# Kernel tuning notes

Hardware: AMD Instinct MI355X
Metric: run time of the kernel (lower is better)

Reference implementation:

```python
import jax, jax.numpy as jnp
import numpy as np

LN_EPS = 1e-6  # flax.linen.LayerNorm default


def setup_inputs() -> dict:
    key = jax.random.key(0)
    ks = jax.random.split(key, 16)
    N_TOT, M = 32768, 12            # total atoms, neighbors per atom
    ORIG, EDGE = 92, 41             # CGCNN atom / edge feature dims
    F, H, L = 128, 256, 3           # atom_fea_len, h_fea_len, n_conv

    def w(k, shape, fan_in):
        return jax.random.normal(k, shape, dtype=jnp.float32) / np.sqrt(fan_in).astype(np.float32)

    return {
        "atom_fea": jax.random.normal(ks[0], (N_TOT, ORIG), dtype=jnp.float32),
        "nbr_fea": jax.random.normal(ks[1], (N_TOT, M, EDGE), dtype=jnp.float32),
        "nbr_fea_idx": jax.random.randint(ks[2], (N_TOT, M), 0, N_TOT),
        # embedding Dense
        "W_embed": w(ks[3], (ORIG, F), ORIG), "b_embed": jnp.zeros((F,), jnp.float32),
        # per-conv-layer stacked params [L, ...]
        "W_center": w(ks[4], (L, F, F), F), "b_center": jnp.zeros((L, F), jnp.float32),
        "W_nbr": w(ks[5], (L, F, F), F), "b_nbr": jnp.zeros((L, F), jnp.float32),
        "W_edge": w(ks[6], (L, EDGE, F), EDGE), "b_edge": jnp.zeros((L, F), jnp.float32),
        "W_gate": w(ks[7], (L, F, F), F), "b_gate": jnp.zeros((L, F), jnp.float32),
        "W_mag": w(ks[8], (L, F, F), F), "b_mag": jnp.zeros((L, F), jnp.float32),
        "ln_scale": jnp.ones((L, F), jnp.float32), "ln_bias": jnp.zeros((L, F), jnp.float32),
        # readout: Dense(h) -> softplus -> Dense(1)
        "W_h": w(ks[9], (F, H), F), "b_h": jnp.zeros((H,), jnp.float32),
        "W_out": w(ks[10], (H, 1), H), "b_out": jnp.zeros((1,), jnp.float32),
        "batch_size": 128,
        "n_atoms_per_crystal": 256,
    }


def _layernorm(x, scale, bias):
    mu = jnp.mean(x, axis=-1, keepdims=True)
    var = jnp.mean(jnp.square(x - mu), axis=-1, keepdims=True)
    return (x - mu) * jax.lax.rsqrt(var + LN_EPS) * scale + bias


def reference(atom_fea, nbr_fea, nbr_fea_idx, W_embed, b_embed,
              W_center, b_center, W_nbr, b_nbr, W_edge, b_edge,
              W_gate, b_gate, W_mag, b_mag, ln_scale, ln_bias,
              W_h, b_h, W_out, b_out, batch_size, n_atoms_per_crystal):
    n_conv = W_center.shape[0]
    x = atom_fea @ W_embed + b_embed                       # [N, F]
    for i in range(n_conv):
        atom_nbr = jnp.take(x, nbr_fea_idx, axis=0)        # [N, M, F] gather
        # Dense on tiled center == Dense on center then broadcast
        phi_c = (x @ W_center[i] + b_center[i])[:, None, :]   # [N, 1, F]
        phi_n = atom_nbr @ W_nbr[i] + b_nbr[i]                # [N, M, F]
        phi_e = nbr_fea @ W_edge[i] + b_edge[i]               # [N, M, F]
        inter = phi_c * phi_n * phi_e                          # [N, M, F]
        gate = jax.nn.sigmoid(inter @ W_gate[i] + b_gate[i])
        mag = jax.nn.softplus(inter @ W_mag[i] + b_mag[i])
        nbr_sumed = jnp.sum(gate * mag, axis=1)               # [N, F]
        x = x + _layernorm(nbr_sumed, ln_scale[i], ln_bias[i])
    E_site = jax.nn.softplus(x @ W_h + b_h) @ W_out + b_out   # [N, 1]
    return jnp.sum(E_site.reshape(batch_size, n_atoms_per_crystal), axis=1, keepdims=True)  # [B, 1]
```

## Files before the change

### kernel.cpp

```cpp
#include <hip/hip_runtime.h>
#include <math.h>

#define N_TOT 32768
#define M_NBR 12
#define ORIG  92
#define EDGE  41
#define FD    128
#define HD    256
#define APC   256
#define NCRY  128

#define STR   136
#define PCS   132
#define WF_PER_LAYER 73728
#define WF_EMBED     12288
#define WF_H         32768

typedef __attribute__((ext_vector_type(8))) short bf16x8;
typedef __attribute__((ext_vector_type(4))) float f32x4;

union BF8 { bf16x8 v; unsigned u[4]; };

__device__ __forceinline__ unsigned pk2(float lo, float hi) {
    unsigned r;
    asm("v_cvt_pk_bf16_f32 %0, %1, %2" : "=v"(r) : "v"(lo), "v"(hi));
    return r;
}
__device__ __forceinline__ short f2bf(float f) { return (short)pk2(f, f); }
__device__ __forceinline__ float bf2f(short s) {
    union { unsigned u; float f; } v; v.u = ((unsigned)(unsigned short)s) << 16;
    return v.f;
}
__device__ __forceinline__ float softplus_f(float x) {
    return fmaxf(x, 0.0f) + 0.6931471805599453f * __log2f(1.0f + __expf(-fabsf(x)));
}
__device__ __forceinline__ float sigmoid_f(float x) {
    return __builtin_amdgcn_rcpf(1.0f + __expf(-x));
}

__global__ __launch_bounds__(256) void swizzle_kernel(
    const float* __restrict__ Wc_all, const float* __restrict__ Wn_all,
    const float* __restrict__ We_all, const float* __restrict__ Wg_all,
    const float* __restrict__ Wm_all, const float* __restrict__ W_embed,
    const float* __restrict__ W_h, short* __restrict__ dst_all)
{
    int gid = blockIdx.x * 256 + threadIdx.x;
    if (gid >= 33280) return;
    const float* W; short* dst; int K_real, fid, stride, l, nt, kt;
    if (gid < 27648) {
        int layer = gid / 9216;
        int rem = gid - layer * 9216;
        short* dbase = dst_all + layer * WF_PER_LAYER;
        if (rem < 2048)      { W = Wc_all + layer * 16384; dst = dbase;         K_real = 128; fid = rem; }
        else if (rem < 4096) { W = Wn_all + layer * 16384; dst = dbase + 16384; K_real = 128; fid = rem - 2048; }
        else if (rem < 5120) { W = We_all + layer * 5248;  dst = dbase + 32768; K_real = 41;  fid = rem - 4096; }
        else if (rem < 7168) { W = Wg_all + layer * 16384; dst = dbase + 40960; K_real = 128; fid = rem - 5120; }
        else                 { W = Wm_all + layer * 16384; dst = dbase + 57344; K_real = 128; fid = rem - 7168; }
        stride = 128; l = fid & 63; nt = (fid >> 6) & 7; kt = fid >> 9;
    } else if (gid < 29184) {
        fid = gid - 27648;
        W = W_embed; dst = dst_all + 3 * WF_PER_LAYER; K_real = ORIG; stride = 128;
        l = fid & 63; nt = (fid >> 6) & 7; kt = fid >> 9;
    } else {
        fid = gid - 29184;
        W = W_h; dst = dst_all + 3 * WF_PER_LAYER + WF_EMBED; K_real = 128; stride = 256;
        l = fid & 63; nt = (fid >> 6) & 15; kt = fid >> 10;
    }
    int n = nt * 16 + (l & 15), kb = kt * 32 + (l >> 4) * 8;
    bf16x8 v;
    #pragma unroll
    for (int j = 0; j < 8; ++j) {
        int k = kb + j;
        v[j] = (k < K_real) ? f2bf(W[k * stride + n]) : (short)0;
    }
    *(bf16x8*)(dst + fid * 8) = v;
}

__global__ __launch_bounds__(256) void embed_mfma_kernel(
    const float* __restrict__ atom_fea, const short* __restrict__ wef,
    const float* __restrict__ b, float* __restrict__ x, short* __restrict__ xbf)
{
    const int tid = threadIdx.x;
    const int w = tid >> 6, lane = tid & 63;
    const int q = lane >> 4, m = lane & 15;
    const int a0 = blockIdx.x * 64;
    const int arow = a0 + w * 16 + m;

    BF8 aA[3];
    const float* ap = atom_fea + (long)arow * ORIG;
    #pragma unroll
    for (int kt = 0; kt < 3; ++kt) {
        const int kb = kt * 32 + q * 8;
        BF8 t;
        if (kb + 7 < ORIG) {
            const float4 u0 = *(const float4*)(ap + kb);
            const float4 u1 = *(const float4*)(ap + kb + 4);
            t.u[0] = pk2(u0.x, u0.y); t.u[1] = pk2(u0.z, u0.w);
            t.u[2] = pk2(u1.x, u1.y); t.u[3] = pk2(u1.z, u1.w);
        } else {
            const float4 u0 = *(const float4*)(ap + kb);
            t.u[0] = pk2(u0.x, u0.y); t.u[1] = pk2(u0.z, u0.w);
            t.u[2] = 0u; t.u[3] = 0u;
        }
        aA[kt] = t;
    }

    #pragma unroll
    for (int ct = 0; ct < 8; ++ct) {
        f32x4 C = {0.f, 0.f, 0.f, 0.f};
        #pragma unroll
        for (int kt = 0; kt < 3; ++kt)
            C = __builtin_amdgcn_mfma_f32_16x16x32_bf16(
                    *(const bf16x8*)(wef + ((kt * 8 + ct) * 64 + lane) * 8), aA[kt].v, C, 0, 0, 0);
        const float4 bv = *(const float4*)(b + ct * 16 + q * 4);
        const float o0 = C[0] + bv.x, o1 = C[1] + bv.y, o2 = C[2] + bv.z, o3 = C[3] + bv.w;
        const long base = ((long)arow << 7) + ct * 16 + q * 4;
        *(float4*)(x + base) = make_float4(o0, o1, o2, o3);
        *(uint2*)(xbf + base) = make_uint2(pk2(o0, o1), pk2(o2, o3));
    }
}

__global__ __launch_bounds__(256) void conv_mfma_kernel(
    const float* __restrict__ x_in, const short* __restrict__ xbf_in,
    float* __restrict__ x_out, short* __restrict__ xbf_out,
    const float* __restrict__ nbr_fea, const int* __restrict__ nbr_idx,
    const short* __restrict__ wf,
    const float* __restrict__ bc, const float* __restrict__ bn,
    const float* __restrict__ be, const float* __restrict__ bg,
    const float* __restrict__ bm,
    const float* __restrict__ lns, const float* __restrict__ lnb)
{
    __shared__ short inter_s[192 * STR];
    __shared__ float phic_s[16 * PCS];
    __shared__ int   idx_s[192];

    const int tid = threadIdx.x;
    const int w = tid >> 6, lane = tid & 63;
    const int q = lane >> 4, m = lane & 15;
    const int a0 = blockIdx.x * 16;
    const long r0 = (long)a0 * M_NBR;

    const short* Wc = wf;
    const short* Wn = wf + 16384;
    const short* We = wf + 32768;
    const short* Wg = wf + 40960;
    const short* Wm = wf + 57344;

    if (tid < 192) idx_s[tid] = nbr_idx[r0 + tid];

    {
        bf16x8 aC[4];
        #pragma unroll
        for (int kt = 0; kt < 4; ++kt)
            aC[kt] = *(const bf16x8*)(xbf_in + ((long)(a0 + m) << 7) + kt * 32 + q * 8);
        #pragma unroll
        for (int ii = 0; ii < 2; ++ii) {
            const int ct = w * 2 + ii;
            f32x4 C = {0.f, 0.f, 0.f, 0.f};
            #pragma unroll
            for (int kt = 0; kt < 4; ++kt)
                C = __builtin_amdgcn_mfma_f32_16x16x32_bf16(
                        *(const bf16x8*)(Wc + ((kt * 8 + ct) * 64 + lane) * 8), aC[kt], C, 0, 0, 0);
            const float4 bv = *(const float4*)(bc + ct * 16 + q * 4);
            *(float4*)(phic_s + m * PCS + ct * 16 + q * 4) =
                make_float4(C[0] + bv.x, C[1] + bv.y, C[2] + bv.z, C[3] + bv.w);
        }
    }
    __syncthreads();

    bf16x8 aN[3][4];
    #pragma unroll
    for (int i = 0; i < 3; ++i) {
        const int row = (w * 3 + i) * 16 + m;
        const long g = (long)idx_s[row] << 7;
        #pragma unroll
        for (int kt = 0; kt < 4; ++kt)
            aN[i][kt] = *(const bf16x8*)(xbf_in + g + kt * 32 + q * 8);
    }
    bf16x8 aE[3][2];
    #pragma unroll
    for (int i = 0; i < 3; ++i) {
        const int row = (w * 3 + i) * 16 + m;
        const float* ep = nbr_fea + (r0 + row) * EDGE;
        BF8 e0, e1;
        const int kb = q * 8;
        e0.u[0] = pk2(ep[kb + 0], ep[kb + 1]);
        e0.u[1] = pk2(ep[kb + 2], ep[kb + 3]);
        e0.u[2] = pk2(ep[kb + 4], ep[kb + 5]);
        e0.u[3] = pk2(ep[kb + 6], ep[kb + 7]);
        e1.u[0] = 0u; e1.u[1] = 0u; e1.u[2] = 0u; e1.u[3] = 0u;
        if (q == 0) {
            e1.u[0] = pk2(ep[32], ep[33]);
            e1.u[1] = pk2(ep[34], ep[35]);
            e1.u[2] = pk2(ep[36], ep[37]);
            e1.u[3] = pk2(ep[38], ep[39]);
        } else if (q == 1) {
            e1.u[0] = pk2(ep[40], 0.0f);
        }
        aE[i][0] = e0.v; aE[i][1] = e1.v;
    }

    int atomL[3];
    #pragma unroll
    for (int i = 0; i < 3; ++i)
        atomL[i] = (w * 48 + i * 16 + m) / 12;

    #pragma unroll
    for (int ct = 0; ct < 8; ++ct) {
        f32x4 Cn[3], Ce[3];
        #pragma unroll
        for (int i = 0; i < 3; ++i) {
            Cn[i] = (f32x4){0.f, 0.f, 0.f, 0.f};
            Ce[i] = (f32x4){0.f, 0.f, 0.f, 0.f};
        }
        #pragma unroll
        for (int kt = 0; kt < 4; ++kt) {
            const bf16x8 nfr = *(const bf16x8*)(Wn + ((kt * 8 + ct) * 64 + lane) * 8);
            #pragma unroll
            for (int i = 0; i < 3; ++i)
                Cn[i] = __builtin_amdgcn_mfma_f32_16x16x32_bf16(nfr, aN[i][kt], Cn[i], 0, 0, 0);
        }
        #pragma unroll
        for (int kt = 0; kt < 2; ++kt) {
            const bf16x8 efr = *(const bf16x8*)(We + ((kt * 8 + ct) * 64 + lane) * 8);
            #pragma unroll
            for (int i = 0; i < 3; ++i)
                Ce[i] = __builtin_amdgcn_mfma_f32_16x16x32_bf16(efr, aE[i][kt], Ce[i], 0, 0, 0);
        }
        const float4 bnv = *(const float4*)(bn + ct * 16 + q * 4);
        const float4 bev = *(const float4*)(be + ct * 16 + q * 4);
        #pragma unroll
        for (int i = 0; i < 3; ++i) {
            const float4 pc = *(const float4*)(phic_s + atomL[i] * PCS + ct * 16 + q * 4);
            const float v0 = pc.x * (Cn[i][0] + bnv.x) * (Ce[i][0] + bev.x);
            const float v1 = pc.y * (Cn[i][1] + bnv.y) * (Ce[i][1] + bev.y);
            const float v2 = pc.z * (Cn[i][2] + bnv.z) * (Ce[i][2] + bev.z);
            const float v3 = pc.w * (Cn[i][3] + bnv.w) * (Ce[i][3] + bev.w);
            *(uint2*)(inter_s + (w * 48 + i * 16 + m) * STR + ct * 16 + q * 4) =
                make_uint2(pk2(v0, v1), pk2(v2, v3));
        }
    }

    bf16x8 aI[3][4];
    #pragma unroll
    for (int i = 0; i < 3; ++i) {
        const int row = (w * 3 + i) * 16 + m;
        #pragma unroll
        for (int kt = 0; kt < 4; ++kt)
            aI[i][kt] = *(const bf16x8*)(inter_s + row * STR + kt * 32 + q * 8);
    }

    #pragma unroll
    for (int ct = 0; ct < 8; ++ct) {
        f32x4 Cg[3], Cm[3];
        #pragma unroll
        for (int i = 0; i < 3; ++i) {
            Cg[i] = (f32x4){0.f, 0.f, 0.f, 0.f};
            Cm[i] = (f32x4){0.f, 0.f, 0.f, 0.f};
        }
        #pragma unroll
        for (int kt = 0; kt < 4; ++kt) {
            const bf16x8 gfr = *(const bf16x8*)(Wg + ((kt * 8 + ct) * 64 + lane) * 8);
            const bf16x8 mfr = *(const bf16x8*)(Wm + ((kt * 8 + ct) * 64 + lane) * 8);
            #pragma unroll
            for (int i = 0; i < 3; ++i) {
                Cg[i] = __builtin_amdgcn_mfma_f32_16x16x32_bf16(gfr, aI[i][kt], Cg[i], 0, 0, 0);
                Cm[i] = __builtin_amdgcn_mfma_f32_16x16x32_bf16(mfr, aI[i][kt], Cm[i], 0, 0, 0);
            }
        }
        const float4 bgv = *(const float4*)(bg + ct * 16 + q * 4);
        const float4 bmv = *(const float4*)(bm + ct * 16 + q * 4);
        #pragma unroll
        for (int i = 0; i < 3; ++i) {
            const float v0 = sigmoid_f(Cg[i][0] + bgv.x) * softplus_f(Cm[i][0] + bmv.x);
            const float v1 = sigmoid_f(Cg[i][1] + bgv.y) * softplus_f(Cm[i][1] + bmv.y);
            const float v2 = sigmoid_f(Cg[i][2] + bgv.z) * softplus_f(Cm[i][2] + bmv.z);
            const float v3 = sigmoid_f(Cg[i][3] + bgv.w) * softplus_f(Cm[i][3] + bmv.w);
            *(uint2*)(inter_s + (w * 48 + i * 16 + m) * STR + ct * 16 + q * 4) =
                make_uint2(pk2(v0, v1), pk2(v2, v3));
        }
    }
    __syncthreads();

    {
        const int a = tid >> 4;
        const int cg = tid & 15;
        float s8[8];
        #pragma unroll
        for (int j = 0; j < 8; ++j) s8[j] = 0.f;
        #pragma unroll
        for (int nb = 0; nb < 12; ++nb) {
            const bf16x8 p = *(const bf16x8*)(inter_s + (a * 12 + nb) * STR + cg * 8);
            #pragma unroll
            for (int j = 0; j < 8; ++j) s8[j] += bf2f(p[j]);
        }
        float lsum = 0.f, lsq = 0.f;
        #pragma unroll
        for (int j = 0; j < 8; ++j) { lsum += s8[j]; lsq += s8[j] * s8[j]; }
        #pragma unroll
        for (int off = 1; off < 16; off <<= 1) {
            lsum += __shfl_xor(lsum, off, 64);
            lsq  += __shfl_xor(lsq,  off, 64);
        }
        const float mu = lsum * (1.0f / FD);
        float var = lsq * (1.0f / FD) - mu * mu;
        var = fmaxf(var, 0.0f);
        const float inv = rsqrtf(var + 1e-6f);
        const long xb = ((long)(a0 + a) << 7) + cg * 8;
        float xv[8], sc[4], sc2[4], bb[4], bb2[4];
        *(float4*)&xv[0] = *(const float4*)(x_in + xb);
        *(float4*)&xv[4] = *(const float4*)(x_in + xb + 4);
        *(float4*)&sc[0]  = *(const float4*)(lns + cg * 8);
        *(float4*)&sc2[0] = *(const float4*)(lns + cg * 8 + 4);
        *(float4*)&bb[0]  = *(const float4*)(lnb + cg * 8);
        *(float4*)&bb2[0] = *(const float4*)(lnb + cg * 8 + 4);
        float o[8];
        #pragma unroll
        for (int j = 0; j < 4; ++j) {
            o[j]     = xv[j]     + (s8[j]     - mu) * inv * sc[j]  + bb[j];
            o[j + 4] = xv[j + 4] + (s8[j + 4] - mu) * inv * sc2[j] + bb2[j];
        }
        BF8 ob;
        ob.u[0] = pk2(o[0], o[1]); ob.u[1] = pk2(o[2], o[3]);
        ob.u[2] = pk2(o[4], o[5]); ob.u[3] = pk2(o[6], o[7]);
        *(float4*)(x_out + xb)     = make_float4(o[0], o[1], o[2], o[3]);
        *(float4*)(x_out + xb + 4) = make_float4(o[4], o[5], o[6], o[7]);
        *(bf16x8*)(xbf_out + xb)   = ob.v;
    }
}

__global__ __launch_bounds__(256) void readout_mfma_kernel(
    const short* __restrict__ xbf, const short* __restrict__ whf,
    const float* __restrict__ bh, const float* __restrict__ Wo,
    const float* __restrict__ bo, float* __restrict__ out)
{
    const int tid = threadIdx.x;
    const int w = tid >> 6, lane = tid & 63;
    const int q = lane >> 4, m = lane & 15;
    const int a0 = blockIdx.x * 64;
    const int arow = a0 + w * 16 + m;

    bf16x8 aX[4];
    #pragma unroll
    for (int kt = 0; kt < 4; ++kt)
        aX[kt] = *(const bf16x8*)(xbf + ((long)arow << 7) + kt * 32 + q * 8);

    float e[4] = {0.f, 0.f, 0.f, 0.f};
    #pragma unroll
    for (int nt = 0; nt < 16; ++nt) {
        f32x4 C = {0.f, 0.f, 0.f, 0.f};
        #pragma unroll
        for (int kt = 0; kt < 4; ++kt)
            C = __builtin_amdgcn_mfma_f32_16x16x32_bf16(
                    aX[kt], *(const bf16x8*)(whf + ((kt * 16 + nt) * 64 + lane) * 8), C, 0, 0, 0);
        const int col = nt * 16 + m;
        const float bhv = bh[col], wov = Wo[col];
        #pragma unroll
        for (int r = 0; r < 4; ++r)
            e[r] += softplus_f(C[r] + bhv) * wov;
    }
    float esum = e[0] + e[1] + e[2] + e[3];
    #pragma unroll
    for (int off = 32; off > 0; off >>= 1)
        esum += __shfl_xor(esum, off, 64);
    if (lane == 0)
        atomicAdd(&out[a0 / APC], esum + 16.0f * bo[0]);
}

__global__ void zero_out_kernel(float* __restrict__ out) {
    if (threadIdx.x < NCRY) out[threadIdx.x] = 0.0f;
}

extern "C" void kernel_launch(void* const* d_in, const int* in_sizes, int n_in,
                              void* d_out, int out_size, void* d_ws, size_t ws_size,
                              hipStream_t stream) {
    const float* atom_fea = (const float*)d_in[0];
    const float* nbr_fea  = (const float*)d_in[1];
    const int*   nbr_idx  = (const int*)d_in[2];
    const float* W_embed  = (const float*)d_in[3];
    const float* b_embed  = (const float*)d_in[4];
    const float* W_center = (const float*)d_in[5];
    const float* b_center = (const float*)d_in[6];
    const float* W_nbr    = (const float*)d_in[7];
    const float* b_nbr    = (const float*)d_in[8];
    const float* W_edge   = (const float*)d_in[9];
    const float* b_edge   = (const float*)d_in[10];
    const float* W_gate   = (const float*)d_in[11];
    const float* b_gate   = (const float*)d_in[12];
    const float* W_mag    = (const float*)d_in[13];
    const float* b_mag    = (const float*)d_in[14];
    const float* ln_scale = (const float*)d_in[15];
    const float* ln_bias  = (const float*)d_in[16];
    const float* W_h      = (const float*)d_in[17];
    const float* b_h      = (const float*)d_in[18];
    const float* W_out    = (const float*)d_in[19];
    const float* b_out    = (const float*)d_in[20];

    float* out = (float*)d_out;
    const size_t NX = (size_t)N_TOT * FD;
    float* xA = (float*)d_ws;
    float* xB = xA + NX;
    short* xbfA = (short*)(xB + NX);
    short* xbfB = xbfA + NX;
    short* wfrag = xbfB + NX;

    swizzle_kernel<<<130, 256, 0, stream>>>(W_center, W_nbr, W_edge, W_gate, W_mag,
                                            W_embed, W_h, wfrag);
    embed_mfma_kernel<<<N_TOT / 64, 256, 0, stream>>>(
        atom_fea, wfrag + 3 * WF_PER_LAYER, b_embed, xA, xbfA);

    const float* xi = xA; float* xo = xB;
    const short* xbi = xbfA; short* xbo = xbfB;
    for (int l = 0; l < 3; ++l) {
        conv_mfma_kernel<<<N_TOT / 16, 256, 0, stream>>>(
            xi, xbi, xo, xbo, nbr_fea, nbr_idx,
            wfrag + (size_t)l * WF_PER_LAYER,
            b_center + (size_t)l * FD, b_nbr + (size_t)l * FD,
            b_edge + (size_t)l * FD, b_gate + (size_t)l * FD,
            b_mag + (size_t)l * FD,
            ln_scale + (size_t)l * FD, ln_bias + (size_t)l * FD);
        const float* tf = xo; xo = (float*)xi; xi = tf;
        const short* tb = xbo; xbo = (short*)xbi; xbi = tb;
    }

    zero_out_kernel<<<1, 128, 0, stream>>>(out);
    readout_mfma_kernel<<<N_TOT / 64, 256, 0, stream>>>(
        xbi, wfrag + 3 * WF_PER_LAYER + WF_EMBED, b_h, W_out, b_out, out);
}
```

Measured before the change: 410.7 us.

## Stream neighbor tiles through per-wave LDS scratch and reduce on the fly

Replaces the 192-row block-wide intermediate buffer with a 16-row scratch tile per wavefront. Each wave now runs the inter, gate and mag GEMMs one 16-row tile at a time and folds the neighbor sum into registers right away. This removes the second block barrier and the separate reduction pass, and it cuts LDS use and live accumulator registers so that four blocks per CU can be requested through launch bounds. Neighbor indices are read straight into registers, and the gather and edge loads are issued before the phi_c GEMM so their latency overlaps it. The cost is more serialized per-tile work inside each wave, and it relies on LDS ordering within a single wave with no explicit barrier.

New measurement: 1.579 ms. 3.85x slower.

```diff
diff --git a/kernel.cpp b/kernel.cpp
--- a/kernel.cpp
+++ b/kernel.cpp
@@ -120,7 +120,7 @@
     }
 }
 
-__global__ __launch_bounds__(256) void conv_mfma_kernel(
+__global__ __launch_bounds__(256, 4) void conv_mfma_kernel(
     const float* __restrict__ x_in, const short* __restrict__ xbf_in,
     float* __restrict__ x_out, short* __restrict__ xbf_out,
     const float* __restrict__ nbr_fea, const int* __restrict__ nbr_idx,
@@ -130,15 +130,15 @@
     const float* __restrict__ bm,
     const float* __restrict__ lns, const float* __restrict__ lnb)
 {
-    __shared__ short inter_s[192 * STR];
+    __shared__ short T_s[4][16 * STR];
     __shared__ float phic_s[16 * PCS];
-    __shared__ int   idx_s[192];
 
     const int tid = threadIdx.x;
     const int w = tid >> 6, lane = tid & 63;
     const int q = lane >> 4, m = lane & 15;
     const int a0 = blockIdx.x * 16;
     const long r0 = (long)a0 * M_NBR;
+    short* T = T_s[w];
 
     const short* Wc = wf;
     const short* Wn = wf + 16384;
@@ -146,41 +146,24 @@
     const short* Wg = wf + 40960;
     const short* Wm = wf + 57344;
 
-    if (tid < 192) idx_s[tid] = nbr_idx[r0 + tid];
-
-    {
-        bf16x8 aC[4];
-        #pragma unroll
-        for (int kt = 0; kt < 4; ++kt)
-            aC[kt] = *(const bf16x8*)(xbf_in + ((long)(a0 + m) << 7) + kt * 32 + q * 8);
-        #pragma unroll
-        for (int ii = 0; ii < 2; ++ii) {
-            const int ct = w * 2 + ii;
-            f32x4 C = {0.f, 0.f, 0.f, 0.f};
-            #pragma unroll
-            for (int kt = 0; kt < 4; ++kt)
-                C = __builtin_amdgcn_mfma_f32_16x16x32_bf16(
-                        *(const bf16x8*)(Wc + ((kt * 8 + ct) * 64 + lane) * 8), aC[kt], C, 0, 0, 0);
-            const float4 bv = *(const float4*)(bc + ct * 16 + q * 4);
-            *(float4*)(phic_s + m * PCS + ct * 16 + q * 4) =
-                make_float4(C[0] + bv.x, C[1] + bv.y, C[2] + bv.z, C[3] + bv.w);
-        }
-    }
-    __syncthreads();
+    int idxv[3];
+    #pragma unroll
+    for (int i = 0; i < 3; ++i)
+        idxv[i] = nbr_idx[r0 + w * 48 + i * 16 + m];
 
     bf16x8 aN[3][4];
     #pragma unroll
     for (int i = 0; i < 3; ++i) {
-        const int row = (w * 3 + i) * 16 + m;
-        const long g = (long)idx_s[row] << 7;
+        const long g = (long)idxv[i] << 7;
         #pragma unroll
         for (int kt = 0; kt < 4; ++kt)
             aN[i][kt] = *(const bf16x8*)(xbf_in + g + kt * 32 + q * 8);
     }
+
     bf16x8 aE[3][2];
     #pragma unroll
     for (int i = 0; i < 3; ++i) {
-        const int row = (w * 3 + i) * 16 + m;
+        const int row = w * 48 + i * 16 + m;
         const float* ep = nbr_fea + (r0 + row) * EDGE;
         BF8 e0, e1;
         const int kb = q * 8;
@@ -200,100 +183,98 @@
         aE[i][0] = e0.v; aE[i][1] = e1.v;
     }
 
+    {
+        bf16x8 aC[4];
+        #pragma unroll
+        for (int kt = 0; kt < 4; ++kt)
+            aC[kt] = *(const bf16x8*)(xbf_in + ((long)(a0 + m) << 7) + kt * 32 + q * 8);
+        #pragma unroll
+        for (int ii = 0; ii < 2; ++ii) {
+            const int ct = w * 2 + ii;
+            f32x4 C = {0.f, 0.f, 0.f, 0.f};
+            #pragma unroll
+            for (int kt = 0; kt < 4; ++kt)
+                C = __builtin_amdgcn_mfma_f32_16x16x32_bf16(
+                        *(const bf16x8*)(Wc + ((kt * 8 + ct) * 64 + lane) * 8), aC[kt], C, 0, 0, 0);
+            const float4 bv = *(const float4*)(bc + ct * 16 + q * 4);
+            *(float4*)(phic_s + m * PCS + ct * 16 + q * 4) =
+                make_float4(C[0] + bv.x, C[1] + bv.y, C[2] + bv.z, C[3] + bv.w);
+        }
+    }
+    __syncthreads();
+
     int atomL[3];
     #pragma unroll
     for (int i = 0; i < 3; ++i)
         atomL[i] = (w * 48 + i * 16 + m) / 12;
 
-    #pragma unroll
-    for (int ct = 0; ct < 8; ++ct) {
-        f32x4 Cn[3], Ce[3];
-        #pragma unroll
-        for (int i = 0; i < 3; ++i) {
-            Cn[i] = (f32x4){0.f, 0.f, 0.f, 0.f};
-            Ce[i] = (f32x4){0.f, 0.f, 0.f, 0.f};
-        }
-        #pragma unroll
-        for (int kt = 0; kt < 4; ++kt) {
-            const bf16x8 nfr = *(const bf16x8*)(Wn + ((kt * 8 + ct) * 64 + lane) * 8);
+    float s8[8];
+    #pragma unroll
+    for (int j = 0; j < 8; ++j) s8[j] = 0.f;
+
+    #pragma unroll
+    for (int i = 0; i < 3; ++i) {
+        #pragma unroll
+        for (int ct = 0; ct < 8; ++ct) {
+            f32x4 Cn = {0.f, 0.f, 0.f, 0.f};
+            f32x4 Ce = {0.f, 0.f, 0.f, 0.f};
             #pragma unroll
-            for (int i = 0; i < 3; ++i)
-                Cn[i] = __builtin_amdgcn_mfma_f32_16x16x32_bf16(nfr, aN[i][kt], Cn[i], 0, 0, 0);
-        }
-        #pragma unroll
-        for (int kt = 0; kt < 2; ++kt) {
-            const bf16x8 efr = *(const bf16x8*)(We + ((kt * 8 + ct) * 64 + lane) * 8);
+            for (int kt = 0; kt < 4; ++kt)
+                Cn = __builtin_amdgcn_mfma_f32_16x16x32_bf16(
+                        *(const bf16x8*)(Wn + ((kt * 8 + ct) * 64 + lane) * 8), aN[i][kt], Cn, 0, 0, 0);
             #pragma unroll
-            for (int i = 0; i < 3; ++i)
-                Ce[i] = __builtin_amdgcn_mfma_f32_16x16x32_bf16(efr, aE[i][kt], Ce[i], 0, 0, 0);
-        }
-        const float4 bnv = *(const float4*)(bn + ct * 16 + q * 4);
-        const float4 bev = *(const float4*)(be + ct * 16 + q * 4);
-        #pragma unroll
-        for (int i = 0; i < 3; ++i) {
-            const float4 pc = *(const float4*)(phic_s + atomL[i] * PCS + ct * 16 + q * 4);
-            const float v0 = pc.x * (Cn[i][0] + bnv.x) * (Ce[i][0] + bev.x);
-            const float v1 = pc.y * (Cn[i][1] + bnv.y) * (Ce[i][1] + bev.y);
-            const float v2 = pc.z * (Cn[i][2] + bnv.z) * (Ce[i][2] + bev.z);
-            const float v3 = pc.w * (Cn[i][3] + bnv.w) * (Ce[i][3] + bev.w);
-            *(uint2*)(inter_s + (w * 48 + i * 16 + m) * STR + ct * 16 + q * 4) =
-                make_uint2(pk2(v0, v1), pk2(v2, v3));
-        }
-    }
-
-    bf16x8 aI[3][4];
-    #pragma unroll
-    for (int i = 0; i < 3; ++i) {
-        const int row = (w * 3 + i) * 16 + m;
+            for (int kt = 0; kt < 2; ++kt)
+                Ce = __builtin_amdgcn_mfma_f32_16x16x32_bf16(
+                        *(const bf16x8*)(We + ((kt * 8 + ct) * 64 + lane) * 8), aE[i][kt], Ce, 0, 0, 0);
+            const float4 bnv = *(const float4*)(bn + ct * 16 + q * 4);
+            const float4 bev = *(const float4*)(be + ct * 16 + q * 4);
+            const float4 pc  = *(const float4*)(phic_s + atomL[i] * PCS + ct * 16 + q * 4);
+            const float v0 = pc.x * (Cn[0] + bnv.x) * (Ce[0] + bev.x);
+            const float v1 = pc.y * (Cn[1] + bnv.y) * (Ce[1] + bev.y);
+            const float v2 = pc.z * (Cn[2] + bnv.z) * (Ce[2] + bev.z);
+            const float v3 = pc.w * (Cn[3] + bnv.w) * (Ce[3] + bev.w);
+            *(uint2*)(T + m * STR + ct * 16 + q * 4) = make_uint2(pk2(v0, v1), pk2(v2, v3));
+        }
+
+        bf16x8 aI[4];
         #pragma unroll
         for (int kt = 0; kt < 4; ++kt)
-            aI[i][kt] = *(const bf16x8*)(inter_s + row * STR + kt * 32 + q * 8);
-    }
-
-    #pragma unroll
-    for (int ct = 0; ct < 8; ++ct) {
-        f32x4 Cg[3], Cm[3];
-        #pragma unroll
-        for (int i = 0; i < 3; ++i) {
-            Cg[i] = (f32x4){0.f, 0.f, 0.f, 0.f};
-            Cm[i] = (f32x4){0.f, 0.f, 0.f, 0.f};
-        }
-        #pragma unroll
-        for (int kt = 0; kt < 4; ++kt) {
-            const bf16x8 gfr = *(const bf16x8*)(Wg + ((kt * 8 + ct) * 64 + lane) * 8);
-            const bf16x8 mfr = *(const bf16x8*)(Wm + ((kt * 8 + ct) * 64 + lane) * 8);
+            aI[kt] = *(const bf16x8*)(T + m * STR + kt * 32 + q * 8);
+
+        #pragma unroll
+        for (int ct = 0; ct < 8; ++ct) {
+            f32x4 Cg = {0.f, 0.f, 0.f, 0.f};
+            f32x4 Cm = {0.f, 0.f, 0.f, 0.f};
             #pragma unroll
-            for (int i = 0; i < 3; ++i) {
-                Cg[i] = __builtin_amdgcn_mfma_f32_16x16x32_bf16(gfr, aI[i][kt], Cg[i], 0, 0, 0);
-                Cm[i] = __builtin_amdgcn_mfma_f32_16x16x32_bf16(mfr, aI[i][kt], Cm[i], 0, 0, 0);
+            for (int kt = 0; kt < 4; ++kt) {
+                Cg = __builtin_amdgcn_mfma_f32_16x16x32_bf16(
+                        *(const bf16x8*)(Wg + ((kt * 8 + ct) * 64 + lane) * 8), aI[kt], Cg, 0, 0, 0);
+                Cm = __builtin_amdgcn_mfma_f32_16x16x32_bf16(
+                        *(const bf16x8*)(Wm + ((kt * 8 + ct) * 64 + lane) * 8), aI[kt], Cm, 0, 0, 0);
             }
-        }
-        const float4 bgv = *(const float4*)(bg + ct * 16 + q * 4);
-        const float4 bmv = *(const float4*)(bm + ct * 16 + q * 4);
-        #pragma unroll
-        for (int i = 0; i < 3; ++i) {
-            const float v0 = sigmoid_f(Cg[i][0] + bgv.x) * softplus_f(Cm[i][0] + bmv.x);
-            const float v1 = sigmoid_f(Cg[i][1] + bgv.y) * softplus_f(Cm[i][1] + bmv.y);
-            const float v2 = sigmoid_f(Cg[i][2] + bgv.z) * softplus_f(Cm[i][2] + bmv.z);
-            const float v3 = sigmoid_f(Cg[i][3] + bgv.w) * softplus_f(Cm[i][3] + bmv.w);
-            *(uint2*)(inter_s + (w * 48 + i * 16 + m) * STR + ct * 16 + q * 4) =
-                make_uint2(pk2(v0, v1), pk2(v2, v3));
-        }
-    }
-    __syncthreads();
+            const float4 bgv = *(const float4*)(bg + ct * 16 + q * 4);
+            const float4 bmv = *(const float4*)(bm + ct * 16 + q * 4);
+            const float v0 = sigmoid_f(Cg[0] + bgv.x) * softplus_f(Cm[0] + bmv.x);
+            const float v1 = sigmoid_f(Cg[1] + bgv.y) * softplus_f(Cm[1] + bmv.y);
+            const float v2 = sigmoid_f(Cg[2] + bgv.z) * softplus_f(Cm[2] + bmv.z);
+            const float v3 = sigmoid_f(Cg[3] + bgv.w) * softplus_f(Cm[3] + bmv.w);
+            *(uint2*)(T + m * STR + ct * 16 + q * 4) = make_uint2(pk2(v0, v1), pk2(v2, v3));
+        }
+
+        {
+            const int lo = max(0, 12 * q - 16 * i);
+            const int hi = min(16, 12 * q + 12 - 16 * i);
+            for (int r2 = lo; r2 < hi; ++r2) {
+                const bf16x8 p = *(const bf16x8*)(T + r2 * STR + m * 8);
+                #pragma unroll
+                for (int j = 0; j < 8; ++j) s8[j] += bf2f(p[j]);
+            }
+        }
+    }
 
     {
         const int a = tid >> 4;
         const int cg = tid & 15;
-        float s8[8];
-        #pragma unroll
-        for (int j = 0; j < 8; ++j) s8[j] = 0.f;
-        #pragma unroll
-        for (int nb = 0; nb < 12; ++nb) {
-            const bf16x8 p = *(const bf16x8*)(inter_s + (a * 12 + nb) * STR + cg * 8);
-            #pragma unroll
-            for (int j = 0; j < 8; ++j) s8[j] += bf2f(p[j]);
-        }
         float lsum = 0.f, lsq = 0.f;
         #pragma unroll
         for (int j = 0; j < 8; ++j) { lsum += s8[j]; lsq += s8[j] * s8[j]; }
```
